# Optimization experiments

Measured on AMD Instinct MI355X. Metric: run time of the kernel, lower is better.

## Reference

```python
import jax, jax.numpy as jnp
import numpy as np

LN_EPS = 1e-5

def layer_norm(x, g, b):
    mu = jnp.mean(x, axis=-1, keepdims=True)
    var = jnp.mean(jnp.square(x - mu), axis=-1, keepdims=True)
    return (x - mu) * jax.lax.rsqrt(var + LN_EPS) * g + b

def ternary_quant(w):
    # BitNet b1.58-style ternary quantization with straight-through estimator
    scale = 1.0 / jnp.clip(jnp.mean(jnp.abs(w)), 1e-5)
    wq = jnp.clip(jnp.round(w * scale), -1.0, 1.0) / scale
    return w + jax.lax.stop_gradient(wq - w)

def setup_inputs() -> dict:
    key = jax.random.key(0)
    ks = jax.random.split(key, 3)
    dim, hidden = 1024, 4096
    B, S = 8, 1024
    x = jax.random.normal(ks[0], (B, S, dim), dtype=jnp.float32)
    w1 = jax.random.normal(ks[1], (hidden, dim), dtype=jnp.float32) * 0.02
    w2 = jax.random.normal(ks[2], (dim, hidden), dtype=jnp.float32) * 0.02
    return {
        "x": x,
        "ln1_g": jnp.ones((dim,), jnp.float32), "ln1_b": jnp.zeros((dim,), jnp.float32),
        "w1": w1, "b1": jnp.zeros((hidden,), jnp.float32),
        "ln2_g": jnp.ones((hidden,), jnp.float32), "ln2_b": jnp.zeros((hidden,), jnp.float32),
        "w2": w2, "b2": jnp.zeros((dim,), jnp.float32),
    }

def reference(x, ln1_g, ln1_b, w1, b1, ln2_g, ln2_b, w2, b2):
    h = layer_norm(x, ln1_g, ln1_b)
    h = jnp.einsum('bsd,hd->bsh', h, ternary_quant(w1)) + b1  # [B,S,hidden]
    h = jax.nn.gelu(h, approximate=False)  # nn.GELU default is exact erf
    h = layer_norm(h, ln2_g, ln2_b)
    out = jnp.einsum('bsh,dh->bsd', h, ternary_quant(w2)) + b2  # [B,S,dim]
    return out
```

## Files before the change

### kernel.cpp

```cpp
#include <hip/hip_runtime.h>
#include <cstdint>
#include <cstddef>

#define DIM   1024
#define HID   4096
#define MROWS 8192

typedef __attribute__((ext_vector_type(8))) __bf16 bf16x8;
typedef __attribute__((ext_vector_type(4))) float  f32x4;
typedef __attribute__((ext_vector_type(4))) int    i32x4;

__device__ __forceinline__ unsigned short f2bf(float f) {
  unsigned int u = __float_as_uint(f);
  u += 0x7fffu + ((u >> 16) & 1u);
  return (unsigned short)(u >> 16);
}
__device__ __forceinline__ float bf2f(unsigned int lo16) {
  return __uint_as_float(lo16 << 16);
}

__device__ __forceinline__ float fast_gelu(float v) {
  float u = v * (0.79788456080286536f + 0.035677408136300125f * v * v);
  float e = __builtin_amdgcn_exp2f(u * 2.8853900817779268f);
  float r = __builtin_amdgcn_rcpf(e + 1.0f);
  return v - v * r;
}

__device__ __forceinline__ void gld16(const void* g, void* l) {
  auto* gp = reinterpret_cast<__attribute__((address_space(1))) unsigned int*>(
      reinterpret_cast<uintptr_t>(g));
  auto* lp = reinterpret_cast<__attribute__((address_space(3))) unsigned int*>(
      reinterpret_cast<uintptr_t>(l));
  __builtin_amdgcn_global_load_lds(gp, lp, 16, 0, 0);
}

__device__ __forceinline__ void wave_reduce2(float& a, float& b) {
#pragma unroll
  for (int off = 32; off > 0; off >>= 1) {
    a += __shfl_xor(a, off, 64);
    b += __shfl_xor(b, off, 64);
  }
}
__device__ __forceinline__ float wave_reduce_max(float m) {
#pragma unroll
  for (int off = 32; off > 0; off >>= 1) m = fmaxf(m, __shfl_xor(m, off, 64));
  return m;
}

__device__ __forceinline__ void block_reduce2(float& a, float& b, int tid) {
  __shared__ float red[8];
  __syncthreads();
  wave_reduce2(a, b);
  if ((tid & 63) == 0) { red[tid >> 6] = a; red[4 + (tid >> 6)] = b; }
  __syncthreads();
  a = red[0] + red[1] + red[2] + red[3];
  b = red[4] + red[5] + red[6] + red[7];
}

__global__ __launch_bounds__(256)
void prep_kernel(const float* __restrict__ w1, const float* __restrict__ w2,
                 float* __restrict__ part,
                 const float* __restrict__ x, const float* __restrict__ g,
                 const float* __restrict__ b, unsigned int* __restrict__ xn8,
                 float* __restrict__ invs) {
  int tid = threadIdx.x;
  int bid = blockIdx.x;
  if (bid < 2048) {
    const float* w = (bid < 1024) ? w1 : w2;
    int blk = bid & 1023;
    const float4* base = (const float4*)w + (size_t)blk * 1024;
    float s = 0.f;
#pragma unroll
    for (int i = 0; i < 4; ++i) {
      float4 v = base[tid + i * 256];
      s += fabsf(v.x) + fabsf(v.y) + fabsf(v.z) + fabsf(v.w);
    }
#pragma unroll
    for (int off = 32; off > 0; off >>= 1) s += __shfl_xor(s, off, 64);
    __shared__ float red[4];
    if ((tid & 63) == 0) red[tid >> 6] = s;
    __syncthreads();
    if (tid == 0) part[bid] = red[0] + red[1] + red[2] + red[3];
  } else {
    const int row  = (bid - 2048) * 4 + (tid >> 6);
    const int lane = tid & 63;
    const float4* xr = (const float4*)(x + (size_t)row * DIM);
    const float4* g4 = (const float4*)g;
    const float4* b4 = (const float4*)b;
    float4 v[4];
    float s = 0.f, ss = 0.f;
#pragma unroll
    for (int p = 0; p < 4; ++p) {
      v[p] = xr[lane + 64 * p];
      s  += v[p].x + v[p].y + v[p].z + v[p].w;
      ss += v[p].x * v[p].x + v[p].y * v[p].y + v[p].z * v[p].z + v[p].w * v[p].w;
    }
    wave_reduce2(s, ss);
    float mu  = s * (1.0f / DIM);
    float var = ss * (1.0f / DIM) - mu * mu;
    float rs  = rsqrtf(var + 1e-5f);
    float n[4][4];
    float amax = 0.f;
#pragma unroll
    for (int p = 0; p < 4; ++p) {
      float4 gg = g4[lane + 64 * p];
      float4 bb = b4[lane + 64 * p];
      n[p][0] = (v[p].x - mu) * rs * gg.x + bb.x;
      n[p][1] = (v[p].y - mu) * rs * gg.y + bb.y;
      n[p][2] = (v[p].z - mu) * rs * gg.z + bb.z;
      n[p][3] = (v[p].w - mu) * rs * gg.w + bb.w;
#pragma unroll
      for (int c = 0; c < 4; ++c) amax = fmaxf(amax, fabsf(n[p][c]));
    }
    amax = wave_reduce_max(amax);
    float sc, iv;
    if (amax < 1e-20f) { sc = 0.f; iv = 0.f; }
    else               { sc = 127.0f / amax; iv = amax * (1.0f / 127.0f); }
    if (lane == 0) invs[row] = iv;
    unsigned int* dst = xn8 + (size_t)row * 256;
#pragma unroll
    for (int p = 0; p < 4; ++p) {
      unsigned r = 0;
#pragma unroll
      for (int c = 0; c < 4; ++c) {
        int q = (int)rintf(n[p][c] * sc);
        r |= ((unsigned)q & 0xffu) << (8 * c);
      }
      dst[lane + 64 * p] = r;
    }
  }
}

__global__ __launch_bounds__(256)
void quant_kernel(const float* __restrict__ part,
                  const float* __restrict__ w1, unsigned int* __restrict__ q1,
                  const float* __restrict__ w2, unsigned short* __restrict__ q2,
                  const float* __restrict__ g2, const float* __restrict__ b2,
                  const float* __restrict__ bias2,
                  float* __restrict__ Sg, float* __restrict__ Cb,
                  float* __restrict__ scal) {
  int bid = blockIdx.x, tid = threadIdx.x;
  const int lane = tid & 63;
  const float4* psrc = (const float4*)(part + ((bid < 512) ? 0 : 1024));
  float a = 0.f, dummy = 0.f;
#pragma unroll
  for (int p = 0; p < 4; ++p) {
    float4 pv = psrc[lane + 64 * p];
    a += pv.x + pv.y + pv.z + pv.w;
  }
  wave_reduce2(a, dummy);
  float mean = fmaxf(a * (1.0f / 4194304.0f), 1e-5f);
  float sc = 1.0f / mean;

  if (bid < 512) {
    if (bid == 0 && tid == 0) scal[0] = mean;
    const int n4 = 1048576;
    int i = bid * 256 + tid;
    for (; i < n4; i += 512 * 256) {
      float4 v = ((const float4*)w1)[i];
      int t0 = (int)fminf(fmaxf(rintf(v.x * sc), -1.f), 1.f);
      int t1 = (int)fminf(fmaxf(rintf(v.y * sc), -1.f), 1.f);
      int t2 = (int)fminf(fmaxf(rintf(v.z * sc), -1.f), 1.f);
      int t3 = (int)fminf(fmaxf(rintf(v.w * sc), -1.f), 1.f);
      unsigned r = ((unsigned)t0 & 0xffu) | (((unsigned)t1 & 0xffu) << 8) |
                   (((unsigned)t2 & 0xffu) << 16) | (((unsigned)t3 & 0xffu) << 24);
      q1[i] = r;
    }
  } else {
    const int d = bid - 512;
    if (d == 0 && tid == 0) scal[1] = mean;
    const float4* wr = (const float4*)(w2 + (size_t)d * HID);
    const float4* g4 = (const float4*)g2;
    const float4* b4 = (const float4*)b2;
    uint2* qr = (uint2*)(q2 + (size_t)d * HID);
    float s1 = 0.f, s2 = 0.f;
#pragma unroll
    for (int i = 0; i < 4; ++i) {
      int idx = tid + 256 * i;
      float4 wv = wr[idx], gv = g4[idx], bv = b4[idx];
      float t0 = fminf(fmaxf(rintf(wv.x * sc), -1.f), 1.f);
      float t1 = fminf(fmaxf(rintf(wv.y * sc), -1.f), 1.f);
      float t2 = fminf(fmaxf(rintf(wv.z * sc), -1.f), 1.f);
      float t3 = fminf(fmaxf(rintf(wv.w * sc), -1.f), 1.f);
      s1 += gv.x * t0 + gv.y * t1 + gv.z * t2 + gv.w * t3;
      s2 += bv.x * t0 + bv.y * t1 + bv.z * t2 + bv.w * t3;
      uint2 r;
      r.x = (unsigned)f2bf(t0 * gv.x) | ((unsigned)f2bf(t1 * gv.y) << 16);
      r.y = (unsigned)f2bf(t2 * gv.z) | ((unsigned)f2bf(t3 * gv.w) << 16);
      qr[idx] = r;
    }
    block_reduce2(s1, s2, tid);
    if (tid == 0) {
      Sg[d] = mean * s1;
      Cb[d] = mean * s2 + bias2[d];
    }
  }
}

__global__ __launch_bounds__(256)
void rowstats_kernel(const unsigned short* __restrict__ h,
                     const float* __restrict__ meanp,
                     float2* __restrict__ murs) {
  const int row  = blockIdx.x * 4 + (threadIdx.x >> 6);
  const int lane = threadIdx.x & 63;
  const uint4* hr = (const uint4*)(h + (size_t)row * HID);
  float s = 0.f, ss = 0.f;
#pragma unroll
  for (int p = 0; p < 8; ++p) {
    uint4 pk = hr[lane + 64 * p];
    const unsigned int* pu = (const unsigned int*)&pk;
#pragma unroll
    for (int j = 0; j < 4; ++j) {
      float lo = bf2f(pu[j] & 0xffffu);
      float hi = __uint_as_float(pu[j] & 0xffff0000u);
      s += lo + hi; ss += lo * lo + hi * hi;
    }
  }
  wave_reduce2(s, ss);
  if (lane == 0) {
    float mu  = s * (1.0f / HID);
    float var = ss * (1.0f / HID) - mu * mu;
    float rs  = rsqrtf(var + 1e-5f);
    murs[row] = make_float2(rs * meanp[1], -rs * mu);
  }
}

__global__ __launch_bounds__(256)
void gemm1_i8(const unsigned char* __restrict__ A,
              const unsigned char* __restrict__ B,
              unsigned short* __restrict__ H,
              const float* __restrict__ wscale_ptr,
              const float* __restrict__ invs,
              const float* __restrict__ bias) {
  __shared__ unsigned char sA[128 * 64];
  __shared__ unsigned char sB[128 * 64];

  const int tid  = threadIdx.x;
  const int lane = tid & 63;
  const int wave = tid >> 6;
  const int wm   = wave & 1;
  const int wn   = wave >> 1;

  const int nbx  = gridDim.x;
  const int id   = blockIdx.y * nbx + blockIdx.x;
  const int xcd  = id & 7;
  const int slot = id >> 3;
  const int bandsPerXcd = gridDim.y >> 3;
  const int band = xcd * bandsPerXcd + slot / nbx;
  const int col  = slot - (slot / nbx) * nbx;
  const int bm   = band * 128;
  const int bn   = col * 128;

  const int csw = ((tid & 3) ^ ((tid >> 3) & 3)) * 16;
  const unsigned char* Ab = A + (size_t)(bm + (tid >> 2)) * 1024 + csw;
  const unsigned char* Bb = B + (size_t)(bn + (tid >> 2)) * 1024 + csw;

  i32x4 acc[4][4] = {};

  const int rowA = (wm * 64 + (lane & 15)) * 64;
  const int rowB = (wn * 64 + (lane & 15)) * 64;
  const int kc = (((lane >> 4) ^ ((lane >> 1) & 3))) * 16;

  for (int k0 = 0; k0 < 1024; k0 += 64) {
    gld16(Ab + k0,              sA + tid * 16);
    gld16(Ab + 64 * 1024 + k0,  sA + 4096 + tid * 16);
    gld16(Bb + k0,              sB + tid * 16);
    gld16(Bb + 64 * 1024 + k0,  sB + 4096 + tid * 16);
    __syncthreads();

    i32x4 af[4], bfr[4];
#pragma unroll
    for (int i = 0; i < 4; ++i) af[i]  = *(const i32x4*)(sA + rowA + i * 1024 + kc);
#pragma unroll
    for (int j = 0; j < 4; ++j) bfr[j] = *(const i32x4*)(sB + rowB + j * 1024 + kc);
#pragma unroll
    for (int i = 0; i < 4; ++i)
#pragma unroll
      for (int j = 0; j < 4; ++j)
        acc[i][j] = __builtin_amdgcn_mfma_i32_16x16x64_i8(af[i], bfr[j], acc[i][j], 0, 0, 0);
    __syncthreads();
  }

  const float wscale = *wscale_ptr;
  float bv[4];
#pragma unroll
  for (int j = 0; j < 4; ++j) bv[j] = bias[bn + wn * 64 + j * 16 + (lane & 15)];
#pragma unroll
  for (int i = 0; i < 4; ++i) {
    const int m0 = bm + wm * 64 + i * 16 + ((lane >> 4) << 2);
    float asc[4];
#pragma unroll
    for (int r = 0; r < 4; ++r) asc[r] = wscale * invs[m0 + r];
#pragma unroll
    for (int j = 0; j < 4; ++j) {
      const int n = bn + wn * 64 + j * 16 + (lane & 15);
#pragma unroll
      for (int r = 0; r < 4; ++r) {
        float v = fast_gelu((float)acc[i][j][r] * asc[r] + bv[j]);
        H[(size_t)(m0 + r) * HID + n] = f2bf(v);
      }
    }
  }
}

__global__ __launch_bounds__(512, 2)
void gemm2_8ph(const unsigned short* __restrict__ A,
               const unsigned short* __restrict__ B,
               float* __restrict__ C,
               const float2* __restrict__ murs,
               const float* __restrict__ Sg,
               const float* __restrict__ Cb) {
  __shared__ unsigned short sA[2][256 * 64];
  __shared__ unsigned short sB[2][128 * 64];

  const int tid  = threadIdx.x;
  const int lane = tid & 63;
  const int wave = tid >> 6;
  const int wm   = wave >> 1;
  const int wn   = wave & 1;

  const int id   = blockIdx.y * 8 + blockIdx.x;
  const int xcd  = id & 7;
  const int slot = id >> 3;
  const int band = xcd * 4 + (slot >> 3);
  const int col  = slot & 7;
  const int bm   = band * 256;
  const int bn   = col * 128;

  const int csw = ((tid & 7) ^ ((tid >> 3) & 7)) << 3;
  const unsigned short* Ab = A + (size_t)(bm + (tid >> 3)) * 4096 + csw;
  const unsigned short* Bb = B + (size_t)(bn + (tid >> 3)) * 4096 + csw;
  char* la0 = (char*)&sA[0][0] + tid * 16;
  char* la1 = (char*)&sA[1][0] + tid * 16;
  char* lb0 = (char*)&sB[0][0] + tid * 16;
  char* lb1 = (char*)&sB[1][0] + tid * 16;

  const int rowAb = (wm * 64 + (lane & 15)) * 128;
  const int rowBb = (wn * 64 + (lane & 15)) * 128;
  const int hi    = lane >> 4;
  const int ck0   = ((hi)     ^ (lane & 7)) << 4;
  const int ck1   = ((hi + 4) ^ (lane & 7)) << 4;

  f32x4 acc[4][4] = {};

#pragma unroll
  for (int i = 0; i < 4; ++i) gld16(Ab + (size_t)i * 262144, la0 + i * 8192);
#pragma unroll
  for (int i = 0; i < 2; ++i) gld16(Bb + (size_t)i * 262144, lb0 + i * 8192);
#pragma unroll
  for (int i = 0; i < 4; ++i) gld16(Ab + (size_t)i * 262144 + 64, la1 + i * 8192);
  asm volatile("s_waitcnt vmcnt(4)" ::: "memory");
  __builtin_amdgcn_s_barrier();

#define Q8(IA, JB)                                                                 \
  do {                                                                             \
    __builtin_amdgcn_s_setprio(1);                                                 \
    _Pragma("unroll") for (int ii = 0; ii < 2; ++ii)                               \
    _Pragma("unroll") for (int jj = 0; jj < 2; ++jj)                               \
    _Pragma("unroll") for (int kk = 0; kk < 2; ++kk)                               \
      acc[IA + ii][JB + jj] = __builtin_amdgcn_mfma_f32_16x16x32_bf16(             \
          af[IA + ii][kk], bfr[JB + jj][kk], acc[IA + ii][JB + jj], 0, 0, 0);      \
    __builtin_amdgcn_s_setprio(0);                                                 \
  } while (0)

  for (int t = 0; t < 64; ++t) {
    const int cur = t & 1;
    const char* a = (const char*)&sA[0][0] + cur * 32768;
    const char* b = (const char*)&sB[0][0] + cur * 16384;
    char* lbP = cur ? lb0 : lb1;
    char* laC = cur ? la1 : la0;
    const size_t kB1 = (t + 1 < 64) ? (size_t)(t + 1) * 64 : 0;
    const size_t kA2 = (t + 2 < 64) ? (size_t)(t + 2) * 64 : 0;

    bf16x8 af[4][2], bfr[4][2];

    af[0][0]  = *(const bf16x8*)(a + rowAb + 0 * 2048 + ck0);
    af[0][1]  = *(const bf16x8*)(a + rowAb + 0 * 2048 + ck1);
    af[1][0]  = *(const bf16x8*)(a + rowAb + 1 * 2048 + ck0);
    af[1][1]  = *(const bf16x8*)(a + rowAb + 1 * 2048 + ck1);
    bfr[0][0] = *(const bf16x8*)(b + rowBb + 0 * 2048 + ck0);
    bfr[0][1] = *(const bf16x8*)(b + rowBb + 0 * 2048 + ck1);
    bfr[1][0] = *(const bf16x8*)(b + rowBb + 1 * 2048 + ck0);
    bfr[1][1] = *(const bf16x8*)(b + rowBb + 1 * 2048 + ck1);
#pragma unroll
    for (int i = 0; i < 2; ++i) gld16(Bb + (size_t)i * 262144 + kB1, lbP + i * 8192);
    __builtin_amdgcn_s_barrier();
    asm volatile("s_waitcnt lgkmcnt(0)" ::: "memory");
    Q8(0, 0);
    __builtin_amdgcn_s_barrier();

    bfr[2][0] = *(const bf16x8*)(b + rowBb + 2 * 2048 + ck0);
    bfr[2][1] = *(const bf16x8*)(b + rowBb + 2 * 2048 + ck1);
    bfr[3][0] = *(const bf16x8*)(b + rowBb + 3 * 2048 + ck0);
    bfr[3][1] = *(const bf16x8*)(b + rowBb + 3 * 2048 + ck1);
    __builtin_amdgcn_s_barrier();
    asm volatile("s_waitcnt lgkmcnt(0)" ::: "memory");
    Q8(0, 2);
    __builtin_amdgcn_s_barrier();

    af[2][0] = *(const bf16x8*)(a + rowAb + 2 * 2048 + ck0);
    af[2][1] = *(const bf16x8*)(a + rowAb + 2 * 2048 + ck1);
    af[3][0] = *(const bf16x8*)(a + rowAb + 3 * 2048 + ck0);
    af[3][1] = *(const bf16x8*)(a + rowAb + 3 * 2048 + ck1);
    __builtin_amdgcn_s_barrier();
    asm volatile("s_waitcnt lgkmcnt(0)" ::: "memory");
    Q8(2, 0);
    __builtin_amdgcn_s_barrier();

#pragma unroll
    for (int i = 0; i < 4; ++i) gld16(Ab + (size_t)i * 262144 + kA2, laC + i * 8192);
    Q8(2, 2);
    asm volatile("s_waitcnt vmcnt(4)" ::: "memory");
    __builtin_amdgcn_s_barrier();
  }
#undef Q8

  asm volatile("s_waitcnt vmcnt(0)" ::: "memory");

  float sg[4], cb[4];
#pragma unroll
  for (int j = 0; j < 4; ++j) {
    const int n = bn + wn * 64 + j * 16 + (lane & 15);
    sg[j] = Sg[n];
    cb[j] = Cb[n];
  }
#pragma unroll
  for (int i = 0; i < 4; ++i) {
    const int m0 = bm + wm * 64 + i * 16 + (hi << 2);
#pragma unroll
    for (int r = 0; r < 4; ++r) {
      float2 ab = murs[m0 + r];
#pragma unroll
      for (int j = 0; j < 4; ++j) {
        const int n = bn + wn * 64 + j * 16 + (lane & 15);
        C[(size_t)(m0 + r) * 1024 + n] = ab.x * acc[i][j][r] + ab.y * sg[j] + cb[j];
      }
    }
  }
}

extern "C" void kernel_launch(void* const* d_in, const int* in_sizes, int n_in,
                              void* d_out, int out_size, void* d_ws, size_t ws_size,
                              hipStream_t stream) {
  const float* x     = (const float*)d_in[0];
  const float* g1    = (const float*)d_in[1];
  const float* b1v   = (const float*)d_in[2];
  const float* w1    = (const float*)d_in[3];
  const float* bias1 = (const float*)d_in[4];
  const float* g2    = (const float*)d_in[5];
  const float* b2v   = (const float*)d_in[6];
  const float* w2    = (const float*)d_in[7];
  const float* bias2 = (const float*)d_in[8];
  float* out = (float*)d_out;

  char* ws = (char*)d_ws;
  float* scal          = (float*)ws;
  float* part          = (float*)(ws + 64);
  float* invs          = (float*)(ws + 16384);
  unsigned int* q1     = (unsigned int*)(ws + 65536);
  unsigned short* q2   = (unsigned short*)(ws + 65536 + 4194304);
  unsigned int* xn8    = (unsigned int*)((char*)q2 + 8388608);
  unsigned short* h    = (unsigned short*)((char*)xn8 + 8388608);
  float2* murs         = (float2*)((char*)h + 67108864);
  float* Sg            = (float*)(murs + 8192);
  float* Cb            = Sg + 1024;

  prep_kernel<<<4096, 256, 0, stream>>>(w1, w2, part, x, g1, b1v, xn8, invs);
  quant_kernel<<<1536, 256, 0, stream>>>(part, w1, q1, w2, q2, g2, b2v, bias2, Sg, Cb, scal);
  gemm1_i8<<<dim3(HID / 128, MROWS / 128), 256, 0, stream>>>(
      (const unsigned char*)xn8, (const unsigned char*)q1, h, scal + 0, invs, bias1);
  rowstats_kernel<<<2048, 256, 0, stream>>>(h, scal, murs);
  gemm2_8ph<<<dim3(8, 32), 512, 0, stream>>>(h, q2, out, murs, Sg, Cb);
}
```

Before: 248.6 us.

## Load GEMM2 A operand directly from global into registers, bypassing LDS

The second GEMM kernel no longer stages the activation (A) tile through shared memory. Each wave now loads its A fragments straight from global memory into double-buffered registers, while B is still staged in LDS. The main loop is restructured into two half-iterations with one barrier each instead of several phase barriers. The aim is to cut LDS traffic and synchronisation, at the cost of more registers and uncoalesced, per-wave duplicated global loads of A that now wait fully on vmcnt(0) every step.

```diff
diff --git a/kernel.cpp b/kernel.cpp
--- a/kernel.cpp
+++ b/kernel.cpp
@@ -304,13 +304,12 @@
 }
 
 __global__ __launch_bounds__(512, 2)
-void gemm2_8ph(const unsigned short* __restrict__ A,
-               const unsigned short* __restrict__ B,
-               float* __restrict__ C,
-               const float2* __restrict__ murs,
-               const float* __restrict__ Sg,
-               const float* __restrict__ Cb) {
-  __shared__ unsigned short sA[2][256 * 64];
+void gemm2_areg(const unsigned short* __restrict__ A,
+                const unsigned short* __restrict__ B,
+                float* __restrict__ C,
+                const float2* __restrict__ murs,
+                const float* __restrict__ Sg,
+                const float* __restrict__ Cb) {
   __shared__ unsigned short sB[2][128 * 64];
 
   const int tid  = threadIdx.x;
@@ -328,94 +327,61 @@
   const int bn   = col * 128;
 
   const int csw = ((tid & 7) ^ ((tid >> 3) & 7)) << 3;
-  const unsigned short* Ab = A + (size_t)(bm + (tid >> 3)) * 4096 + csw;
   const unsigned short* Bb = B + (size_t)(bn + (tid >> 3)) * 4096 + csw;
-  char* la0 = (char*)&sA[0][0] + tid * 16;
-  char* la1 = (char*)&sA[1][0] + tid * 16;
   char* lb0 = (char*)&sB[0][0] + tid * 16;
   char* lb1 = (char*)&sB[1][0] + tid * 16;
 
-  const int rowAb = (wm * 64 + (lane & 15)) * 128;
   const int rowBb = (wn * 64 + (lane & 15)) * 128;
   const int hi    = lane >> 4;
   const int ck0   = ((hi)     ^ (lane & 7)) << 4;
   const int ck1   = ((hi + 4) ^ (lane & 7)) << 4;
 
+  const unsigned short* aBase =
+      A + (size_t)(bm + wm * 64 + (lane & 15)) * 4096 + (hi << 3);
+
   f32x4 acc[4][4] = {};
-
-#pragma unroll
-  for (int i = 0; i < 4; ++i) gld16(Ab + (size_t)i * 262144, la0 + i * 8192);
+  bf16x8 afA[4][2], afB[4][2];
+
 #pragma unroll
   for (int i = 0; i < 2; ++i) gld16(Bb + (size_t)i * 262144, lb0 + i * 8192);
 #pragma unroll
-  for (int i = 0; i < 4; ++i) gld16(Ab + (size_t)i * 262144 + 64, la1 + i * 8192);
-  asm volatile("s_waitcnt vmcnt(4)" ::: "memory");
+  for (int i = 0; i < 4; ++i)
+#pragma unroll
+    for (int s = 0; s < 2; ++s)
+      afA[i][s] = *(const bf16x8*)(aBase + i * 65536 + s * 32);
+  asm volatile("s_waitcnt vmcnt(0)" ::: "memory");
   __builtin_amdgcn_s_barrier();
 
-#define Q8(IA, JB)                                                                 \
-  do {                                                                             \
-    __builtin_amdgcn_s_setprio(1);                                                 \
-    _Pragma("unroll") for (int ii = 0; ii < 2; ++ii)                               \
-    _Pragma("unroll") for (int jj = 0; jj < 2; ++jj)                               \
-    _Pragma("unroll") for (int kk = 0; kk < 2; ++kk)                               \
-      acc[IA + ii][JB + jj] = __builtin_amdgcn_mfma_f32_16x16x32_bf16(             \
-          af[IA + ii][kk], bfr[JB + jj][kk], acc[IA + ii][JB + jj], 0, 0, 0);      \
-    __builtin_amdgcn_s_setprio(0);                                                 \
+#define HALF_ITER(AF_CUR, AF_NXT, CUR, LB_NXT, KNXT)                            \
+  do {                                                                          \
+    const size_t kn = (KNXT);                                                   \
+    _Pragma("unroll") for (int i = 0; i < 2; ++i)                               \
+      gld16(Bb + (size_t)i * 262144 + kn, (LB_NXT) + i * 8192);                 \
+    _Pragma("unroll") for (int i = 0; i < 4; ++i)                               \
+    _Pragma("unroll") for (int s = 0; s < 2; ++s)                               \
+      AF_NXT[i][s] = *(const bf16x8*)(aBase + i * 65536 + kn + s * 32);         \
+    bf16x8 bfr[4][2];                                                           \
+    const char* bp = (const char*)&sB[0][0] + (CUR) * 16384;                    \
+    _Pragma("unroll") for (int j = 0; j < 4; ++j) {                             \
+      bfr[j][0] = *(const bf16x8*)(bp + rowBb + j * 2048 + ck0);                \
+      bfr[j][1] = *(const bf16x8*)(bp + rowBb + j * 2048 + ck1);                \
+    }                                                                           \
+    __builtin_amdgcn_s_setprio(1);                                              \
+    _Pragma("unroll") for (int i2 = 0; i2 < 4; ++i2)                            \
+    _Pragma("unroll") for (int j2 = 0; j2 < 4; ++j2)                            \
+    _Pragma("unroll") for (int kk = 0; kk < 2; ++kk)                            \
+      acc[i2][j2] = __builtin_amdgcn_mfma_f32_16x16x32_bf16(                    \
+          AF_CUR[i2][kk], bfr[j2][kk], acc[i2][j2], 0, 0, 0);                   \
+    __builtin_amdgcn_s_setprio(0);                                              \
+    asm volatile("s_waitcnt vmcnt(0)" ::: "memory");                            \
+    __builtin_amdgcn_s_barrier();                                               \
   } while (0)
 
-  for (int t = 0; t < 64; ++t) {
-    const int cur = t & 1;
-    const char* a = (const char*)&sA[0][0] + cur * 32768;
-    const char* b = (const char*)&sB[0][0] + cur * 16384;
-    char* lbP = cur ? lb0 : lb1;
-    char* laC = cur ? la1 : la0;
-    const size_t kB1 = (t + 1 < 64) ? (size_t)(t + 1) * 64 : 0;
-    const size_t kA2 = (t + 2 < 64) ? (size_t)(t + 2) * 64 : 0;
-
-    bf16x8 af[4][2], bfr[4][2];
-
-    af[0][0]  = *(const bf16x8*)(a + rowAb + 0 * 2048 + ck0);
-    af[0][1]  = *(const bf16x8*)(a + rowAb + 0 * 2048 + ck1);
-    af[1][0]  = *(const bf16x8*)(a + rowAb + 1 * 2048 + ck0);
-    af[1][1]  = *(const bf16x8*)(a + rowAb + 1 * 2048 + ck1);
-    bfr[0][0] = *(const bf16x8*)(b + rowBb + 0 * 2048 + ck0);
-    bfr[0][1] = *(const bf16x8*)(b + rowBb + 0 * 2048 + ck1);
-    bfr[1][0] = *(const bf16x8*)(b + rowBb + 1 * 2048 + ck0);
-    bfr[1][1] = *(const bf16x8*)(b + rowBb + 1 * 2048 + ck1);
-#pragma unroll
-    for (int i = 0; i < 2; ++i) gld16(Bb + (size_t)i * 262144 + kB1, lbP + i * 8192);
-    __builtin_amdgcn_s_barrier();
-    asm volatile("s_waitcnt lgkmcnt(0)" ::: "memory");
-    Q8(0, 0);
-    __builtin_amdgcn_s_barrier();
-
-    bfr[2][0] = *(const bf16x8*)(b + rowBb + 2 * 2048 + ck0);
-    bfr[2][1] = *(const bf16x8*)(b + rowBb + 2 * 2048 + ck1);
-    bfr[3][0] = *(const bf16x8*)(b + rowBb + 3 * 2048 + ck0);
-    bfr[3][1] = *(const bf16x8*)(b + rowBb + 3 * 2048 + ck1);
-    __builtin_amdgcn_s_barrier();
-    asm volatile("s_waitcnt lgkmcnt(0)" ::: "memory");
-    Q8(0, 2);
-    __builtin_amdgcn_s_barrier();
-
-    af[2][0] = *(const bf16x8*)(a + rowAb + 2 * 2048 + ck0);
-    af[2][1] = *(const bf16x8*)(a + rowAb + 2 * 2048 + ck1);
-    af[3][0] = *(const bf16x8*)(a + rowAb + 3 * 2048 + ck0);
-    af[3][1] = *(const bf16x8*)(a + rowAb + 3 * 2048 + ck1);
-    __builtin_amdgcn_s_barrier();
-    asm volatile("s_waitcnt lgkmcnt(0)" ::: "memory");
-    Q8(2, 0);
-    __builtin_amdgcn_s_barrier();
-
-#pragma unroll
-    for (int i = 0; i < 4; ++i) gld16(Ab + (size_t)i * 262144 + kA2, laC + i * 8192);
-    Q8(2, 2);
-    asm volatile("s_waitcnt vmcnt(4)" ::: "memory");
-    __builtin_amdgcn_s_barrier();
-  }
-#undef Q8
-
-  asm volatile("s_waitcnt vmcnt(0)" ::: "memory");
+  for (int t = 0; t < 64; t += 2) {
+    HALF_ITER(afA, afB, 0, lb1, (size_t)(t + 1) * 64);
+    HALF_ITER(afB, afA, 1, lb0, (t + 2 < 64) ? (size_t)(t + 2) * 64 : 0);
+  }
+#undef HALF_ITER
 
   float sg[4], cb[4];
 #pragma unroll
@@ -470,5 +436,5 @@
   gemm1_i8<<<dim3(HID / 128, MROWS / 128), 256, 0, stream>>>(
       (const unsigned char*)xn8, (const unsigned char*)q1, h, scal + 0, invs, bias1);
   rowstats_kernel<<<2048, 256, 0, stream>>>(h, scal, murs);
-  gemm2_8ph<<<dim3(8, 32), 512, 0, stream>>>(h, q2, out, murs, Sg, Cb);
-}
+  gemm2_areg<<<dim3(8, 32), 512, 0, stream>>>(h, q2, out, murs, Sg, Cb);
+}
```

New measurement: 337.8 us. 1.36x slower.
